# Kernel optimization log

Measured on AMD Instinct MI355X. Metric: run time of the kernel, lower is better.

Reference implementation:

```python
import jax, jax.numpy as jnp
import numpy as np

N_E, N_R, E = 100000, 1000, 1000000
E_HID, R_HID = 128, 128
NEG_SLOPE = 0.01


def _seg_softmax(logits, seg, num_segments):
    # torch_geometric.utils.softmax: per-segment max-subtracted softmax, +1e-16 in denom
    m = jax.ops.segment_max(logits, seg, num_segments=num_segments)
    m = jnp.where(jnp.isfinite(m), m, 0.0)  # empty segments
    z = jnp.exp(logits - m[seg])
    s = jax.ops.segment_sum(z, seg, num_segments=num_segments)
    return z / (s[seg] + 1e-16)


def setup_inputs() -> dict:
    key = jax.random.key(0)
    ks = jax.random.split(key, 10)
    s_e = 1.0 / np.sqrt(E_HID)
    s_r = 1.0 / np.sqrt(R_HID)
    s_2r = 1.0 / np.sqrt(2 * R_HID)
    return {
        "x_e": jax.random.normal(ks[0], (N_E, E_HID), jnp.float32),
        "x_r": jax.random.normal(ks[1], (N_R, R_HID), jnp.float32),
        "edge_index": jax.random.randint(ks[2], (2, E), 0, N_E, jnp.int32),
        "rel": jax.random.randint(ks[3], (E,), 0, N_R, jnp.int32),
        "rel_all": jax.random.randint(ks[4], (N_R,), 0, N_R, jnp.int32),
        "w_ah": jax.random.uniform(ks[5], (E_HID,), jnp.float32, -s_e, s_e),
        "w_at": jax.random.uniform(ks[6], (E_HID,), jnp.float32, -s_e, s_e),
        "w_ar": jax.random.uniform(ks[7], (R_HID,), jnp.float32, -s_r, s_r),
        "W_r1": jax.random.uniform(ks[8], (R_HID, 2 * R_HID), jnp.float32, -s_r, s_r),
        "b_r1": jnp.zeros((2 * R_HID,), jnp.float32),
        "W_r2": jax.random.uniform(ks[9], (2 * R_HID, R_HID), jnp.float32, -s_2r, s_2r),
        "b_r2": jnp.zeros((R_HID,), jnp.float32),
        "W_r": jax.random.uniform(jax.random.fold_in(key, 99), (2 * R_HID, 2 * R_HID), jnp.float32, -s_2r, s_2r),
        "b_r": jnp.zeros((2 * R_HID,), jnp.float32),
    }


def reference(x_e, x_r, edge_index, rel, rel_all, w_ah, w_at, w_ar,
              W_r1, b_r1, W_r2, b_r2, W_r, b_r):
    h, t = edge_index[0], edge_index[1]
    n_e = x_e.shape[0]

    # per-node/per-rel attention scores, gathered per edge
    e_h = (x_e @ w_ah)[h]          # [E]
    e_t = (x_e @ w_at)[t]          # [E]
    e_r = (x_r @ w_ar)[rel]        # [E]

    alpha_h = _seg_softmax(jax.nn.leaky_relu(e_h + e_r, NEG_SLOPE), h, n_e)
    alpha_t = _seg_softmax(jax.nn.leaky_relu(e_t + e_r, NEG_SLOPE), t, n_e)

    # relation transform (no activation in original)
    x_r2 = (x_r @ W_r1 + b_r1) @ W_r2 + b_r2   # [N_r, r_hidden]
    msg = x_r + x_r2                            # [N_r, r_hidden]

    # sparse.mm(adj, msg) == weighted scatter-add over edges
    msg_e = msg[rel]                            # [E, r_hidden]
    x_e_h = jax.ops.segment_sum(alpha_h[:, None] * msg_e, h, num_segments=n_e)
    x_e_t = jax.ops.segment_sum(alpha_t[:, None] * msg_e, t, num_segments=n_e)

    x = jnp.concatenate([x_e_h, x_e_t], axis=1)  # [N_e, 2*r_hidden]
    return x @ W_r + b_r
```

## Files before the change

kernel.cpp:

```cpp
#include <hip/hip_runtime.h>
#include <hip/hip_fp16.h>


#define CH1    2048
#define SUPW   4096
#define CAP1   45056
#define CH2    4096
#define CHUNK2 (CAP1 / CH2)
#define NBPS   128
#define CAP2   512
#define MAXD   64
#define NSB    2048

#define MIX_LO(acc, w, z) \
    asm("v_fma_mix_f32 %0, %1, %2, %0 op_sel:[0,0,0] op_sel_hi:[1,0,0]" \
        : "+v"(acc) : "v"(w), "v"(z))
#define MIX_HI(acc, w, z) \
    asm("v_fma_mix_f32 %0, %1, %2, %0 op_sel:[1,0,0] op_sel_hi:[1,0,0]" \
        : "+v"(acc) : "v"(w), "v"(z))

__device__ __forceinline__ float dot4(float4 a, float4 b) {
    return a.x * b.x + a.y * b.y + a.z * b.z + a.w * b.w;
}

__global__ __launch_bounds__(256) void k_front(
    const float* __restrict__ xe, const float* __restrict__ xr,
    const float* __restrict__ wah, const float* __restrict__ wat, const float* __restrict__ war,
    const float* __restrict__ W1, const float* __restrict__ b1,
    const float* __restrict__ W2, const float* __restrict__ b2,
    const float* __restrict__ Wr,
    const int* __restrict__ ei,
    float* __restrict__ eh, float* __restrict__ et, float* __restrict__ er,
    __half* __restrict__ Mh, __half* __restrict__ Mt,
    int* __restrict__ hist,
    int nE, int nR, int E, int nH, int nSR) {
    __shared__ float xs[128];
    __shared__ float hs[256];
    __shared__ float ms[128];
    __shared__ int cnt[64];
    int b = blockIdx.x, tid = threadIdx.x;
    int lane = tid & 63;
    if (b < nR) {
        int r = b, j = tid;
        if (j < 128) xs[j] = xr[(size_t)r * 128 + j];
        __syncthreads();
        {
            float acc = b1[j];
            #pragma unroll 8
            for (int k = 0; k < 128; ++k) acc += xs[k] * W1[k * 256 + j];
            hs[j] = acc;
        }
        __syncthreads();
        if (j < 128) {
            float acc = b2[j] + xs[j];
            #pragma unroll 8
            for (int k = 0; k < 256; ++k) acc += hs[k] * W2[k * 128 + j];
            ms[j] = acc;
        }
        __syncthreads();
        {
            float ah = 0.f, at_ = 0.f;
            #pragma unroll 8
            for (int i = 0; i < 128; ++i) {
                float m = ms[i];
                ah  += m * Wr[i * 256 + j];
                at_ += m * Wr[(128 + i) * 256 + j];
            }
            Mh[(size_t)r * 256 + j] = __float2half(ah);
            Mt[(size_t)r * 256 + j] = __float2half(at_);
        }
    } else if (b < nR + nH) {
        int blk = b - nR;
        if (tid < 64) cnt[tid] = 0;
        __syncthreads();
        int base = blk * CH1;
        #pragma unroll
        for (int k = 0; k < CH1 / 256; ++k) {
            int e = base + k * 256 + tid;
            if (e < E) {
                unsigned vh = ((unsigned)ei[e]) << 1;
                unsigned vt = (((unsigned)ei[E + e]) << 1) | 1u;
                atomicAdd(&cnt[vh >> 12], 1);
                atomicAdd(&cnt[vt >> 12], 1);
            }
        }
        __syncthreads();
        if (tid < 64) hist[tid * 512 + blk] = cnt[tid];
    } else if (b < nR + nH + nSR) {
        int row = (b - nR - nH) * 32 + (tid >> 6) * 8 + (lane >> 3);
        int seg = lane & 7;
        if (row < nR) {
            const float4* xp = (const float4*)(xr + (size_t)row * 128 + seg * 16);
            const float4* cp = (const float4*)(war + seg * 16);
            float d = 0.f;
            #pragma unroll
            for (int q = 0; q < 4; ++q) d += dot4(xp[q], cp[q]);
            #pragma unroll
            for (int m = 4; m >= 1; m >>= 1) d += __shfl_xor(d, m);
            if (seg == 0) er[row] = d;
        }
    } else {
        int sb = b - nR - nH - nSR;
        int rowInTile = (tid >> 6) * 8 + (lane >> 3);
        int seg = lane & 7;
        const float4* ap = (const float4*)(wah + seg * 16);
        const float4* bp = (const float4*)(wat + seg * 16);
        float4 a0 = ap[0], a1 = ap[1], a2 = ap[2], a3 = ap[3];
        float4 b0 = bp[0], b1_ = bp[1], b2_ = bp[2], b3 = bp[3];
        int row0 = sb * 32 + rowInTile;
        int row1 = row0 + NSB * 32;
        int r1c = min(row1, nE - 1);
        const float4* p0 = (const float4*)(xe + (size_t)row0 * 128 + seg * 16);
        const float4* p1 = (const float4*)(xe + (size_t)r1c * 128 + seg * 16);
        float4 u0 = p0[0], u1 = p0[1], u2 = p0[2], u3 = p0[3];
        float4 w0 = p1[0], w1 = p1[1], w2 = p1[2], w3 = p1[3];
        float dh0 = dot4(u0, a0) + dot4(u1, a1) + dot4(u2, a2) + dot4(u3, a3);
        float dt0 = dot4(u0, b0) + dot4(u1, b1_) + dot4(u2, b2_) + dot4(u3, b3);
        float dh1 = dot4(w0, a0) + dot4(w1, a1) + dot4(w2, a2) + dot4(w3, a3);
        float dt1 = dot4(w0, b0) + dot4(w1, b1_) + dot4(w2, b2_) + dot4(w3, b3);
        #pragma unroll
        for (int m = 4; m >= 1; m >>= 1) {
            dh0 += __shfl_xor(dh0, m); dt0 += __shfl_xor(dt0, m);
            dh1 += __shfl_xor(dh1, m); dt1 += __shfl_xor(dt1, m);
        }
        if (seg == 0) {
            eh[row0] = dh0; et[row0] = dt0;
            if (row1 < nE) { eh[row1] = dh1; et[row1] = dt1; }
        }
    }
}

__global__ __launch_bounds__(256) void k_scanp(
    int* __restrict__ hist, int* __restrict__ bcur1,
    int* __restrict__ bcur2, int nbuck, int nblk) {
    __shared__ int wtot[4];
    int bin = blockIdx.x, tid = threadIdx.x, lane = tid & 63, wid = tid >> 6;
    for (int g = bin * 256 + tid; g < nbuck; g += 64 * 256) bcur2[g] = 0;
    int j0 = 2 * tid, j1 = 2 * tid + 1;
    int v0 = (j0 < nblk) ? hist[bin * 512 + j0] : 0;
    int v1 = (j1 < nblk) ? hist[bin * 512 + j1] : 0;
    int ts = v0 + v1;
    int incl = ts;
    #pragma unroll
    for (int d = 1; d < 64; d <<= 1) { int u = __shfl_up(incl, d); if (lane >= d) incl += u; }
    if (lane == 63) wtot[wid] = incl;
    __syncthreads();
    int wbase = 0;
    for (int w = 0; w < wid; ++w) wbase += wtot[w];
    int excl = wbase + incl - ts;
    hist[bin * 512 + j0] = excl;
    hist[bin * 512 + j1] = excl + v0;
    if (tid == 255) bcur1[bin] = wbase + incl;
}

__global__ __launch_bounds__(256) void k_part1(
    const int* __restrict__ ei, const int* __restrict__ rel,
    const int* __restrict__ hist, unsigned* __restrict__ part1, int E) {
    __shared__ unsigned stage[CH1 * 2];
    __shared__ int cnt[64], offs_[64], cur[64], gb[64];
    int tid = threadIdx.x;
    if (tid < 64) cnt[tid] = 0;
    __syncthreads();
    int base = blockIdx.x * CH1;
    unsigned wh[CH1 / 256], wt[CH1 / 256];
    bool ve[CH1 / 256];
    #pragma unroll
    for (int k = 0; k < CH1 / 256; ++k) {
        int e = base + k * 256 + tid;
        ve[k] = (e < E);
        unsigned h = 0, t = 0, r = 0;
        if (ve[k]) { h = (unsigned)ei[e]; t = (unsigned)ei[E + e]; r = (unsigned)rel[e]; }
        unsigned vh = h << 1, vt = (t << 1) | 1u;
        wh[k] = ((vh >> 12) << 26) | ((vh & 4095u) << 10) | r;
        wt[k] = ((vt >> 12) << 26) | ((vt & 4095u) << 10) | r;
        if (ve[k]) { atomicAdd(&cnt[wh[k] >> 26], 1); atomicAdd(&cnt[wt[k] >> 26], 1); }
    }
    __syncthreads();
    if (tid < 64) {
        int v = cnt[tid], incl = v;
        #pragma unroll
        for (int d = 1; d < 64; d <<= 1) { int u = __shfl_up(incl, d); if (tid >= d) incl += u; }
        offs_[tid] = incl - v;
        cur[tid] = incl - v;
        gb[tid] = hist[tid * 512 + blockIdx.x];
    }
    __syncthreads();
    #pragma unroll
    for (int k = 0; k < CH1 / 256; ++k) {
        if (ve[k]) {
            int p = atomicAdd(&cur[wh[k] >> 26], 1); stage[p] = wh[k];
            int q = atomicAdd(&cur[wt[k] >> 26], 1); stage[q] = wt[k];
        }
    }
    __syncthreads();
    int total = offs_[63] + cnt[63];
    for (int p = tid; p < total; p += 256) {
        unsigned w = stage[p];
        int bin = w >> 26;
        int dst = gb[bin] + (p - offs_[bin]);
        if (dst < CAP1) part1[(size_t)bin * CAP1 + dst] = w & 0x03FFFFFFu;
    }
}

__global__ __launch_bounds__(256) void k_part2(
    const int* __restrict__ bcur1, const unsigned* __restrict__ part1,
    int* __restrict__ bcur2, unsigned short* __restrict__ part2) {
    int s = blockIdx.x / CHUNK2, c = blockIdx.x % CHUNK2;
    int cnt_s = min(bcur1[s], CAP1);
    int start = c * CH2;
    if (start >= cnt_s) return;
    __shared__ unsigned stage[CH2];
    __shared__ int cnt[NBPS], offs_[NBPS], cur[NBPS], gb[NBPS];
    __shared__ int wt2[2];
    int tid = threadIdx.x;
    if (tid < NBPS) cnt[tid] = 0;
    __syncthreads();
    unsigned w_[CH2 / 256];
    bool v_[CH2 / 256];
    #pragma unroll
    for (int k = 0; k < CH2 / 256; ++k) {
        int i = start + k * 256 + tid;
        v_[k] = (i < cnt_s);
        unsigned it = v_[k] ? part1[(size_t)s * CAP1 + i] : 0u;
        unsigned sb = ((it >> 10) & 4095u) >> 5;
        unsigned entry = (((it >> 10) & 31u) << 10) | (it & 1023u);
        w_[k] = (sb << 16) | entry;
        if (v_[k]) atomicAdd(&cnt[sb], 1);
    }
    __syncthreads();
    int v128 = 0, incl128 = 0;
    if (tid < NBPS) {
        v128 = cnt[tid]; incl128 = v128;
        int lane = tid & 63;
        #pragma unroll
        for (int d = 1; d < 64; d <<= 1) { int u = __shfl_up(incl128, d); if (lane >= d) incl128 += u; }
        if (lane == 63) wt2[tid >> 6] = incl128;
    }
    __syncthreads();
    if (tid < NBPS) {
        int base2 = (tid >= 64) ? wt2[0] : 0;
        int excl = base2 + incl128 - v128;
        offs_[tid] = excl;
        cur[tid] = excl;
        gb[tid] = atomicAdd(&bcur2[s * NBPS + tid], v128);
    }
    __syncthreads();
    #pragma unroll
    for (int k = 0; k < CH2 / 256; ++k)
        if (v_[k]) { int p = atomicAdd(&cur[w_[k] >> 16], 1); stage[p] = w_[k]; }
    __syncthreads();
    int total = offs_[NBPS - 1] + cnt[NBPS - 1];
    for (int p = tid; p < total; p += 256) {
        unsigned w = stage[p];
        int sb = w >> 16;
        int dst = gb[sb] + (p - offs_[sb]);
        if (dst < CAP2) part2[((size_t)s * NBPS + sb) * CAP2 + dst] = (unsigned short)w;
    }
}

__global__ __launch_bounds__(256) void k_group_out10(
    const int* __restrict__ bcur2, const unsigned short* __restrict__ part2,
    const float* __restrict__ eh, const float* __restrict__ et, const float* __restrict__ er,
    const __half* __restrict__ Mh, const __half* __restrict__ Mt,
    const float* __restrict__ br, float* __restrict__ out, int nE, int nR) {
    __shared__ unsigned short csr[CAP2];
    __shared__ float er_s[1024];
    __shared__ unsigned zbufZ[4][2][64];
    __shared__ unsigned zbufO[4][2][64];
    __shared__ int cnt[32], offs_[32], cur[32];
    int b = blockIdx.x, tid = threadIdx.x;
    int count = min(bcur2[b], CAP2);
    unsigned mtOff = (unsigned)nR * 512u;
    if (tid < 32) cnt[tid] = 0;
    for (int i = tid; i < nR; i += 256) er_s[i] = er[i];
    __syncthreads();
    unsigned short ev[CAP2 / 256];
    bool val[CAP2 / 256];
    #pragma unroll
    for (int k = 0; k < CAP2 / 256; ++k) {
        int i = tid + k * 256;
        val[k] = (i < count);
        ev[k] = val[k] ? part2[(size_t)b * CAP2 + i] : (unsigned short)0;
        if (val[k]) atomicAdd(&cnt[ev[k] >> 10], 1);
    }
    __syncthreads();
    if (tid < 32) {
        int v = cnt[tid], incl = v;
        #pragma unroll
        for (int d = 1; d < 32; d <<= 1) { int u = __shfl_up(incl, d); if (tid >= d) incl += u; }
        offs_[tid] = incl - v;
        cur[tid] = incl - v;
    }
    __syncthreads();
    #pragma unroll
    for (int k = 0; k < CAP2 / 256; ++k) {
        if (val[k]) {
            int p = atomicAdd(&cur[ev[k] >> 10], 1);
            csr[p] = (unsigned short)(ev[k] & 1023u);
        }
    }
    __syncthreads();
    int lane = tid & 63, wid = tid >> 6;
    int half = lane >> 5, l31 = lane & 31;
    unsigned loff = (unsigned)(l31 << 4);
    const char* Mbase = (const char*)Mh;
    float4 bv = *(const float4*)(br + l31 * 8 + half * 4);
    int nbase = b * 16;
    for (int li = wid; li < 16; li += 4) {
        int n = nbase + li;
        if (n >= nE) break;
        int oH = offs_[2 * li];
        int oT = offs_[2 * li + 1];
        int dH = min(cur[2 * li] - oH, MAXD);
        int dT = min(cur[2 * li + 1] - oT, MAXD);
        float ehn = eh[n], etn = et[n];
        unsigned zHv = 0u, oHv = 0u;
        unsigned zTv = 0u, oTv = mtOff;
        if (lane < dH) {
            int r = csr[oH + lane];
            float l = ehn + er_s[r]; l = l > 0.f ? l : 0.01f * l;
            zHv = __float_as_uint(__expf(l)) & 0xFFFFFC00u;
            oHv = (unsigned)r << 9;
        }
        if (lane < dT) {
            int r = csr[oT + lane];
            float l = etn + er_s[r]; l = l > 0.f ? l : 0.01f * l;
            zTv = __float_as_uint(__expf(l)) & 0xFFFFFC00u;
            oTv = ((unsigned)r << 9) + mtOff;
        }
        zbufZ[wid][0][lane] = zHv; zbufO[wid][0][lane] = oHv;
        zbufZ[wid][1][lane] = zTv; zbufO[wid][1][lane] = oTv;
        const unsigned* zrowZ = &zbufZ[wid][half][0];
        const unsigned* zrowO = &zbufO[wid][half][0];
        float acc[8] = {0, 0, 0, 0, 0, 0, 0, 0};
        float s = 0.f;
        int kk = (max(dH, dT) + 3) & ~3;
        for (int j = 0; j < kk; j += 4) {
            uint4 z4 = *(const uint4*)(zrowZ + j);
            uint4 o4 = *(const uint4*)(zrowO + j);
            unsigned za[4] = {z4.x, z4.y, z4.z, z4.w};
            unsigned oa[4] = {o4.x, o4.y, o4.z, o4.w};
            #pragma unroll
            for (int i = 0; i < 4; ++i) {
                float z = __uint_as_float(za[i]);
                uint4 m = *(const uint4*)(Mbase + (oa[i] + loff));
                MIX_LO(acc[0], m.x, z); MIX_HI(acc[1], m.x, z);
                MIX_LO(acc[2], m.y, z); MIX_HI(acc[3], m.y, z);
                MIX_LO(acc[4], m.z, z); MIX_HI(acc[5], m.z, z);
                MIX_LO(acc[6], m.w, z); MIX_HI(acc[7], m.w, z);
                s += z;
            }
        }
        float sO = __shfl_xor(s, 32);
        float iMine = 1.f / (s + 1e-16f);
        float iOther = 1.f / (sO + 1e-16f);
        float oq[4];
        #pragma unroll
        for (int q = 0; q < 4; ++q) {
            float send = half ? acc[q] : acc[4 + q];
            float mine = half ? acc[4 + q] : acc[q];
            float recv = __shfl_xor(send, 32);
            oq[q] = mine * iMine + recv * iOther;
        }
        float4 o;
        o.x = oq[0] + bv.x;
        o.y = oq[1] + bv.y;
        o.z = oq[2] + bv.z;
        o.w = oq[3] + bv.w;
        *(float4*)(out + (size_t)n * 256 + l31 * 8 + half * 4) = o;
    }
}

__global__ __launch_bounds__(256) void k_scores(
    const float* __restrict__ xe, const float* __restrict__ xr,
    const float* __restrict__ wah, const float* __restrict__ wat, const float* __restrict__ war,
    float* __restrict__ eh, float* __restrict__ et, float* __restrict__ er,
    int nE, int nR) {
    int wid = (blockIdx.x * blockDim.x + threadIdx.x) >> 6;
    int lane = threadIdx.x & 63;
    if (wid < nE) {
        float2 x2 = *(const float2*)(xe + (size_t)wid * 128 + lane * 2);
        float2 a2 = *(const float2*)(wah + lane * 2);
        float2 b2 = *(const float2*)(wat + lane * 2);
        float dh = x2.x * a2.x + x2.y * a2.y;
        float dt = x2.x * b2.x + x2.y * b2.y;
        #pragma unroll
        for (int m = 32; m >= 1; m >>= 1) { dh += __shfl_xor(dh, m); dt += __shfl_xor(dt, m); }
        if (lane == 0) { eh[wid] = dh; et[wid] = dt; }
    } else if (wid < nE + nR) {
        int r = wid - nE;
        float2 x2 = *(const float2*)(xr + (size_t)r * 128 + lane * 2);
        float2 c2 = *(const float2*)(war + lane * 2);
        float d = x2.x * c2.x + x2.y * c2.y;
        #pragma unroll
        for (int m = 32; m >= 1; m >>= 1) d += __shfl_xor(d, m);
        if (lane == 0) er[r] = d;
    }
}

__global__ __launch_bounds__(256) void k_rel(
    const float* __restrict__ xr,
    const float* __restrict__ W1, const float* __restrict__ b1,
    const float* __restrict__ W2, const float* __restrict__ b2,
    const float* __restrict__ Wr,
    __half* __restrict__ Mh, __half* __restrict__ Mt) {
    __shared__ float xs[128];
    __shared__ float hs[256];
    __shared__ float ms[128];
    int r = blockIdx.x, j = threadIdx.x;
    if (j < 128) xs[j] = xr[(size_t)r * 128 + j];
    __syncthreads();
    {
        float acc = b1[j];
        #pragma unroll 4
        for (int k = 0; k < 128; ++k) acc += xs[k] * W1[k * 256 + j];
        hs[j] = acc;
    }
    __syncthreads();
    if (j < 128) {
        float acc = b2[j] + xs[j];
        #pragma unroll 4
        for (int k = 0; k < 256; ++k) acc += hs[k] * W2[k * 128 + j];
        ms[j] = acc;
    }
    __syncthreads();
    {
        float ah = 0.f, at_ = 0.f;
        #pragma unroll 4
        for (int i = 0; i < 128; ++i) {
            float m = ms[i];
            ah  += m * Wr[i * 256 + j];
            at_ += m * Wr[(128 + i) * 256 + j];
        }
        Mh[(size_t)r * 256 + j] = __float2half(ah);
        Mt[(size_t)r * 256 + j] = __float2half(at_);
    }
}

__global__ __launch_bounds__(256) void k_hist(
    const int* __restrict__ ei, int* __restrict__ deg, int E, int nE) {
    int e = blockIdx.x * blockDim.x + threadIdx.x;
    if (e >= E) return;
    atomicAdd(&deg[ei[e]], 1);
    atomicAdd(&deg[nE + ei[E + e]], 1);
}

__global__ __launch_bounds__(256) void k_scan1(
    const int* __restrict__ deg, int* __restrict__ offs, int* __restrict__ bsum, int N) {
    __shared__ int wtot[4];
    int tid = threadIdx.x, lane = tid & 63, wid = tid >> 6;
    int base = blockIdx.x * 1024 + tid * 4;
    int v[4];
    #pragma unroll
    for (int i = 0; i < 4; ++i) v[i] = (base + i < N) ? deg[base + i] : 0;
    int ts = v[0] + v[1] + v[2] + v[3];
    int incl = ts;
    #pragma unroll
    for (int d = 1; d < 64; d <<= 1) { int u = __shfl_up(incl, d); if (lane >= d) incl += u; }
    if (lane == 63) wtot[wid] = incl;
    __syncthreads();
    int wbase = 0;
    for (int w = 0; w < wid; ++w) wbase += wtot[w];
    int run = wbase + incl - ts;
    #pragma unroll
    for (int i = 0; i < 4; ++i) { if (base + i < N) offs[base + i] = run; run += v[i]; }
    if (tid == 255) bsum[blockIdx.x] = wbase + incl;
}

__global__ __launch_bounds__(256) void k_scan2(int* __restrict__ bsum, int NB) {
    __shared__ int wtot[4];
    int tid = threadIdx.x, lane = tid & 63, wid = tid >> 6;
    int v = (tid < NB) ? bsum[tid] : 0;
    int incl = v;
    #pragma unroll
    for (int d = 1; d < 64; d <<= 1) { int u = __shfl_up(incl, d); if (lane >= d) incl += u; }
    if (lane == 63) wtot[wid] = incl;
    __syncthreads();
    int wbase = 0;
    for (int w = 0; w < wid; ++w) wbase += wtot[w];
    if (tid < NB) bsum[tid] = wbase + incl - v;
}

__global__ __launch_bounds__(256) void k_scan3(
    int* __restrict__ offs, const int* __restrict__ bsum, int* __restrict__ cursor, int N) {
    int i = blockIdx.x * blockDim.x + threadIdx.x;
    if (i >= N) return;
    int v = offs[i] + bsum[i >> 10];
    offs[i] = v;
    cursor[i] = v;
}

__global__ __launch_bounds__(256) void k_scatter_offs(
    const int* __restrict__ ei, const int* __restrict__ rel,
    const float* __restrict__ eh, const float* __restrict__ et, const float* __restrict__ er,
    int* __restrict__ cursor, unsigned* __restrict__ csr, int E, int nE) {
    int e = blockIdx.x * blockDim.x + threadIdx.x;
    if (e >= E) return;
    int h = ei[e], t = ei[E + e], r = rel[e];
    float erv = er[r];
    float lh = eh[h] + erv; lh = lh > 0.f ? lh : 0.01f * lh;
    float lt = et[t] + erv; lt = lt > 0.f ? lt : 0.01f * lt;
    unsigned zh = (__float_as_uint(__expf(lh)) & 0xFFFFFC00u) | (unsigned)r;
    unsigned zt = (__float_as_uint(__expf(lt)) & 0xFFFFFC00u) | (unsigned)r;
    int ph = atomicAdd(&cursor[h], 1);
    csr[ph] = zh;
    int pt = atomicAdd(&cursor[nE + t], 1);
    csr[pt] = zt;
}

__global__ __launch_bounds__(256) void k_out_offs(
    const int* __restrict__ offs, const int* __restrict__ deg, const unsigned* __restrict__ csr,
    const __half* __restrict__ Mh, const __half* __restrict__ Mt, const float* __restrict__ br,
    float* __restrict__ out, int nE) {
    int wid = (blockIdx.x * blockDim.x + threadIdx.x) >> 6;
    int lane = threadIdx.x & 63;
    if (wid >= nE) return;
    int dH = deg[wid], dT = deg[nE + wid];
    size_t offH = (size_t)offs[wid], offT = (size_t)offs[nE + wid];
    float4 accH = {0, 0, 0, 0}, accT = {0, 0, 0, 0};
    float sH = 0.f, sT = 0.f;
    int dM = max(dH, dT);
    for (int b = 0; b < dM; b += 64) {
        int kH = min(64, dH - b);
        int kT = min(64, dT - b);
        unsigned eH = 0, eT = 0;
        if (lane < kH) eH = csr[offH + b + lane];
        if (lane < kT) eT = csr[offT + b + lane];
        int kk = max(kH, kT);
        for (int j = 0; j < kk; ++j) {
            unsigned cH = (unsigned)__shfl((int)eH, j);
            unsigned cT = (unsigned)__shfl((int)eT, j);
            if (j < kH) {
                float z = __uint_as_float(cH & 0xFFFFFC00u);
                int r = (int)(cH & 0x3FFu);
                const __half2* mp = (const __half2*)(Mh + ((size_t)r << 8) + (lane << 2));
                float2 m01 = __half22float2(mp[0]);
                float2 m23 = __half22float2(mp[1]);
                accH.x += z * m01.x; accH.y += z * m01.y;
                accH.z += z * m23.x; accH.w += z * m23.y;
                sH += z;
            }
            if (j < kT) {
                float z = __uint_as_float(cT & 0xFFFFFC00u);
                int r = (int)(cT & 0x3FFu);
                const __half2* mp = (const __half2*)(Mt + ((size_t)r << 8) + (lane << 2));
                float2 m01 = __half22float2(mp[0]);
                float2 m23 = __half22float2(mp[1]);
                accT.x += z * m01.x; accT.y += z * m01.y;
                accT.z += z * m23.x; accT.w += z * m23.y;
                sT += z;
            }
        }
    }
    float iH = 1.f / (sH + 1e-16f);
    float iT = 1.f / (sT + 1e-16f);
    float4 bv = *(const float4*)(br + lane * 4);
    float4 o;
    o.x = accH.x * iH + accT.x * iT + bv.x;
    o.y = accH.y * iH + accT.y * iT + bv.y;
    o.z = accH.z * iH + accT.z * iT + bv.z;
    o.w = accH.w * iH + accT.w * iT + bv.w;
    *(float4*)(out + (size_t)wid * 256 + lane * 4) = o;
}

extern "C" void kernel_launch(void* const* d_in, const int* in_sizes, int n_in,
                              void* d_out, int out_size, void* d_ws, size_t ws_size,
                              hipStream_t stream) {
    const float* xe  = (const float*)d_in[0];
    const float* xr  = (const float*)d_in[1];
    const int*   ei  = (const int*)d_in[2];
    const int*   rel = (const int*)d_in[3];
    const float* wah = (const float*)d_in[5];
    const float* wat = (const float*)d_in[6];
    const float* war = (const float*)d_in[7];
    const float* W1  = (const float*)d_in[8];
    const float* b1  = (const float*)d_in[9];
    const float* W2  = (const float*)d_in[10];
    const float* b2  = (const float*)d_in[11];
    const float* Wr  = (const float*)d_in[12];
    const float* br  = (const float*)d_in[13];
    float* out = (float*)d_out;

    const int nE = in_sizes[0] / 128;
    const int nR = in_sizes[1] / 128;
    const int E  = in_sizes[3];
    const int N  = 2 * nE;
    const int NSUP  = (N + SUPW - 1) / SUPW;
    const int NBUCK = NSUP * NBPS;
    const int NBLK1 = (E + CH1 - 1) / CH1;
    const int NSR   = (nR + 31) / 32;

    float* ws = (float*)d_ws;
    size_t o = 0;
    auto alloc = [&](size_t words) { size_t r = o; o += (words + 3) & ~(size_t)3; return r; };
    float* eh     = ws + alloc(nE);
    float* et     = ws + alloc(nE);
    float* er     = ws + alloc(nR);
    __half* Mh    = (__half*)(ws + alloc((size_t)nR * 128));
    __half* Mt    = (__half*)(ws + alloc((size_t)nR * 128));
    size_t common_words = o;

    size_t hist_words  = 64 * 512;
    size_t part1_words = (size_t)NSUP * CAP1;
    size_t part2_words = ((size_t)NBUCK * CAP2 + 1) / 2;
    size_t new_words = hist_words + 64 + NBUCK + part1_words + part2_words;
    bool planNew = (NBLK1 <= 512) && (NSUP <= 64) && (nE >= NSB * 32) &&
                   (ws_size >= (common_words + new_words + 64) * 4);

    if (planNew) {
        int* hist   = (int*)(ws + alloc(hist_words));
        int* bcur1  = (int*)(ws + alloc(64));
        int* bcur2  = (int*)(ws + alloc(NBUCK));
        unsigned* part1 = (unsigned*)(ws + alloc(part1_words));
        unsigned short* part2 = (unsigned short*)(ws + alloc(part2_words));
        k_front<<<nR + NBLK1 + NSR + NSB, 256, 0, stream>>>(
            xe, xr, wah, wat, war, W1, b1, W2, b2, Wr, ei,
            eh, et, er, Mh, Mt, hist, nE, nR, E, NBLK1, NSR);
        k_scanp<<<64, 256, 0, stream>>>(hist, bcur1, bcur2, NBUCK, NBLK1);
        k_part1<<<NBLK1, 256, 0, stream>>>(ei, rel, hist, part1, E);
        k_part2<<<NSUP * CHUNK2, 256, 0, stream>>>(bcur1, part1, bcur2, part2);
        k_group_out10<<<NBUCK, 256, 0, stream>>>(bcur2, part2, eh, et, er, Mh, Mt, br, out, nE, nR);
    } else {
        int* cursor = (int*)(ws + alloc(N));
        int* deg    = (int*)(ws + alloc(N));
        int* offs   = (int*)(ws + alloc(N));
        int* bsum   = (int*)(ws + alloc(512));
        unsigned* csr = (unsigned*)(ws + alloc(2 * (size_t)E));
        const int NB = (N + 1023) / 1024;
        k_scores<<<(nE + nR + 3) / 4, 256, 0, stream>>>(xe, xr, wah, wat, war, eh, et, er, nE, nR);
        k_rel<<<nR, 256, 0, stream>>>(xr, W1, b1, W2, b2, Wr, Mh, Mt);
        hipMemsetAsync(deg, 0, (size_t)N * sizeof(int), stream);
        k_hist<<<(E + 255) / 256, 256, 0, stream>>>(ei, deg, E, nE);
        k_scan1<<<NB, 256, 0, stream>>>(deg, offs, bsum, N);
        k_scan2<<<1, 256, 0, stream>>>(bsum, NB);
        k_scan3<<<(N + 255) / 256, 256, 0, stream>>>(offs, bsum, cursor, N);
        k_scatter_offs<<<(E + 255) / 256, 256, 0, stream>>>(ei, rel, eh, et, er, cursor, csr, E, nE);
        k_out_offs<<<(nE + 3) / 4, 256, 0, stream>>>(offs, deg, csr, Mh, Mt, br, out, nE);
    }
}
```

Before: 267.6 us.

## Fold histogram prefix scan into partition kernels and drop separate scan launch

```diff
diff --git a/kernel.cpp b/kernel.cpp
--- a/kernel.cpp
+++ b/kernel.cpp
@@ -46,14 +46,14 @@
         __syncthreads();
         {
             float acc = b1[j];
-            #pragma unroll 8
+            #pragma unroll 16
             for (int k = 0; k < 128; ++k) acc += xs[k] * W1[k * 256 + j];
             hs[j] = acc;
         }
         __syncthreads();
         if (j < 128) {
             float acc = b2[j] + xs[j];
-            #pragma unroll 8
+            #pragma unroll 16
             for (int k = 0; k < 256; ++k) acc += hs[k] * W2[k * 128 + j];
             ms[j] = acc;
         }
@@ -130,38 +130,27 @@
     }
 }
 
-__global__ __launch_bounds__(256) void k_scanp(
-    int* __restrict__ hist, int* __restrict__ bcur1,
-    int* __restrict__ bcur2, int nbuck, int nblk) {
-    __shared__ int wtot[4];
-    int bin = blockIdx.x, tid = threadIdx.x, lane = tid & 63, wid = tid >> 6;
-    for (int g = bin * 256 + tid; g < nbuck; g += 64 * 256) bcur2[g] = 0;
-    int j0 = 2 * tid, j1 = 2 * tid + 1;
-    int v0 = (j0 < nblk) ? hist[bin * 512 + j0] : 0;
-    int v1 = (j1 < nblk) ? hist[bin * 512 + j1] : 0;
-    int ts = v0 + v1;
-    int incl = ts;
-    #pragma unroll
-    for (int d = 1; d < 64; d <<= 1) { int u = __shfl_up(incl, d); if (lane >= d) incl += u; }
-    if (lane == 63) wtot[wid] = incl;
-    __syncthreads();
-    int wbase = 0;
-    for (int w = 0; w < wid; ++w) wbase += wtot[w];
-    int excl = wbase + incl - ts;
-    hist[bin * 512 + j0] = excl;
-    hist[bin * 512 + j1] = excl + v0;
-    if (tid == 255) bcur1[bin] = wbase + incl;
-}
-
 __global__ __launch_bounds__(256) void k_part1(
     const int* __restrict__ ei, const int* __restrict__ rel,
-    const int* __restrict__ hist, unsigned* __restrict__ part1, int E) {
+    const int* __restrict__ hist, unsigned* __restrict__ part1,
+    int* __restrict__ bcur2, int E, int nbuck) {
     __shared__ unsigned stage[CH1 * 2];
     __shared__ int cnt[64], offs_[64], cur[64], gb[64];
-    int tid = threadIdx.x;
+    __shared__ int psum[4][64];
+    int tid = threadIdx.x, myb = blockIdx.x;
+    int g0 = myb * 256 + tid;
+    if (g0 < nbuck) bcur2[g0] = 0;
+    {
+        int bin = tid & 63, q = tid >> 6;
+        int per = (myb + 3) >> 2;
+        int lo = q * per, hi = min(lo + per, myb);
+        int s = 0;
+        for (int j = lo; j < hi; ++j) s += hist[bin * 512 + j];
+        psum[q][bin] = s;
+    }
     if (tid < 64) cnt[tid] = 0;
     __syncthreads();
-    int base = blockIdx.x * CH1;
+    int base = myb * CH1;
     unsigned wh[CH1 / 256], wt[CH1 / 256];
     bool ve[CH1 / 256];
     #pragma unroll
@@ -182,7 +171,7 @@
         for (int d = 1; d < 64; d <<= 1) { int u = __shfl_up(incl, d); if (tid >= d) incl += u; }
         offs_[tid] = incl - v;
         cur[tid] = incl - v;
-        gb[tid] = hist[tid * 512 + blockIdx.x];
+        gb[tid] = psum[0][tid] + psum[1][tid] + psum[2][tid] + psum[3][tid];
     }
     __syncthreads();
     #pragma unroll
@@ -203,16 +192,25 @@
 }
 
 __global__ __launch_bounds__(256) void k_part2(
-    const int* __restrict__ bcur1, const unsigned* __restrict__ part1,
-    int* __restrict__ bcur2, unsigned short* __restrict__ part2) {
+    const int* __restrict__ hist, const unsigned* __restrict__ part1,
+    int* __restrict__ bcur2, unsigned short* __restrict__ part2, int nblk) {
     int s = blockIdx.x / CHUNK2, c = blockIdx.x % CHUNK2;
-    int cnt_s = min(bcur1[s], CAP1);
+    __shared__ int totS;
+    int tid = threadIdx.x;
+    if (tid == 0) totS = 0;
+    __syncthreads();
+    {
+        int part = 0;
+        for (int j = tid; j < nblk; j += 256) part += hist[s * 512 + j];
+        atomicAdd(&totS, part);
+    }
+    __syncthreads();
+    int cnt_s = min(totS, CAP1);
     int start = c * CH2;
     if (start >= cnt_s) return;
     __shared__ unsigned stage[CH2];
     __shared__ int cnt[NBPS], offs_[NBPS], cur[NBPS], gb[NBPS];
     __shared__ int wt2[2];
-    int tid = threadIdx.x;
     if (tid < NBPS) cnt[tid] = 0;
     __syncthreads();
     unsigned w_[CH2 / 256];
@@ -613,12 +611,12 @@
         int* bcur2  = (int*)(ws + alloc(NBUCK));
         unsigned* part1 = (unsigned*)(ws + alloc(part1_words));
         unsigned short* part2 = (unsigned short*)(ws + alloc(part2_words));
+        (void)bcur1;
         k_front<<<nR + NBLK1 + NSR + NSB, 256, 0, stream>>>(
             xe, xr, wah, wat, war, W1, b1, W2, b2, Wr, ei,
             eh, et, er, Mh, Mt, hist, nE, nR, E, NBLK1, NSR);
-        k_scanp<<<64, 256, 0, stream>>>(hist, bcur1, bcur2, NBUCK, NBLK1);
-        k_part1<<<NBLK1, 256, 0, stream>>>(ei, rel, hist, part1, E);
-        k_part2<<<NSUP * CHUNK2, 256, 0, stream>>>(bcur1, part1, bcur2, part2);
+        k_part1<<<NBLK1, 256, 0, stream>>>(ei, rel, hist, part1, bcur2, E, NBUCK);
+        k_part2<<<NSUP * CHUNK2, 256, 0, stream>>>(hist, part1, bcur2, part2, NBLK1);
         k_group_out10<<<NBUCK, 256, 0, stream>>>(bcur2, part2, eh, et, er, Mh, Mt, br, out, nE, nR);
     } else {
         int* cursor = (int*)(ws + alloc(N));
```

Result: slower. 277.1 us (+3.6%).
